# Performance work log

Hardware: AMD Instinct MI355X
Metric: run time of the kernel (lower is better)

## Reference

```python
import jax, jax.numpy as jnp
from jax import lax
import numpy as np

N, D, K, T, E, S = 2048, 128, 16, 16, 8192, 256
GAMMA, SIGMA, TEMP, EPS = 0.1, 1.0, 1.0, 1e-10


def _xavier(k, out_d, in_d):
    lim = (6.0 / (in_d + out_d)) ** 0.5
    return jax.random.uniform(k, (out_d, in_d), minval=-lim, maxval=lim, dtype=jnp.float32)


def setup_inputs() -> dict:
    key = jax.random.key(0)
    ks = jax.random.split(key, 24)
    inp = {
        'edges': jax.random.randint(ks[0], (T, E, 2), 0, N, dtype=jnp.int32),
        'subject_idx': 3,
        'eps_phi': jax.random.normal(ks[1], (T, N, D), dtype=jnp.float32),
        'eps_beta': jax.random.normal(ks[2], (T, K, D), dtype=jnp.float32),
        'u_gumbel': jax.random.uniform(ks[3], (T, 2 * E, K), dtype=jnp.float32),
        'alpha_mean_emb': jax.random.normal(ks[4], (S, D), dtype=jnp.float32),
        'alpha_std_emb': jax.random.normal(ks[5], (S, D), dtype=jnp.float32),
        'W_s2phi': _xavier(ks[6], N * D, D), 'b_s2phi': jnp.zeros((N * D,), jnp.float32),
        'W_s2beta': _xavier(ks[7], K * D, D), 'b_s2beta': jnp.zeros((K * D,), jnp.float32),
        'W_bmean': _xavier(ks[8], D, D), 'b_bmean': jnp.zeros((D,), jnp.float32),
        'W_bstd': _xavier(ks[9], D, D), 'b_bstd': jnp.zeros((D,), jnp.float32),
        'W_pmean': _xavier(ks[10], D, D), 'b_pmean': jnp.zeros((D,), jnp.float32),
        'W_pstd': _xavier(ks[11], D, D), 'b_pstd': jnp.zeros((D,), jnp.float32),
        'W_pi': _xavier(ks[12], K, D),
        'Wih_n': 0.1 * jax.random.normal(ks[13], (3 * D, 2 * D), dtype=jnp.float32),
        'Whh_n': 0.1 * jax.random.normal(ks[14], (3 * D, D), dtype=jnp.float32),
        'bih_n': jnp.zeros((3 * D,), jnp.float32), 'bhh_n': jnp.zeros((3 * D,), jnp.float32),
        'Wih_c': 0.1 * jax.random.normal(ks[15], (3 * D, 2 * D), dtype=jnp.float32),
        'Whh_c': 0.1 * jax.random.normal(ks[16], (3 * D, D), dtype=jnp.float32),
        'bih_c': jnp.zeros((3 * D,), jnp.float32), 'bhh_c': jnp.zeros((3 * D,), jnp.float32),
        'W_dec': _xavier(ks[17], N, D),
    }
    return inp


def _gru(x, h, Wih, Whh, bih, bhh):
    # torch nn.GRU single-step cell (gate order r, z, n)
    gi = x @ Wih.T + bih
    gh = h @ Whh.T + bhh
    i_r, i_z, i_n = jnp.split(gi, 3, axis=-1)
    h_r, h_z, h_n = jnp.split(gh, 3, axis=-1)
    r = jax.nn.sigmoid(i_r + h_r)
    z = jax.nn.sigmoid(i_z + h_z)
    n = jnp.tanh(i_n + r * h_n)
    return (1.0 - z) * n + z * h


def _kld_gauss(m1, s1, m2, s2):
    # KL(N(m1,s1) || N(m2,s2)), s2 scalar
    return 0.5 * jnp.sum(2.0 * (jnp.log(s2) - jnp.log(s1)) + (s1 ** 2 + (m1 - m2) ** 2) / (s2 ** 2) - 1.0)


def reference(edges, subject_idx, eps_phi, eps_beta, u_gumbel,
              alpha_mean_emb, alpha_std_emb, W_s2phi, b_s2phi, W_s2beta, b_s2beta,
              W_bmean, b_bmean, W_bstd, b_bstd, W_pmean, b_pmean, W_pstd, b_pstd,
              W_pi, Wih_n, Whh_n, bih_n, bhh_n, Wih_c, Whh_c, bih_c, bhh_c, W_dec):
    a_m = alpha_mean_emb[subject_idx]
    a_s = jax.nn.softplus(alpha_std_emb[subject_idx])
    kld_alpha = _kld_gauss(a_m, a_s, jnp.zeros_like(a_m), 1.0)
    phi0 = (a_m @ W_s2phi.T + b_s2phi).reshape(N, D)
    beta0 = (a_m @ W_s2beta.T + b_s2beta).reshape(K, D)

    def step(carry, xs):
        h_phi, h_beta, phi_prior, beta_prior = carry
        e_t, ep, eb, u = xs
        w = jnp.concatenate([e_t[:, 0], e_t[:, 1]])  # [2E]
        c = jnp.concatenate([e_t[:, 1], e_t[:, 0]])  # [2E]
        h_phi = _gru(jnp.concatenate([phi_prior, phi_prior], -1), h_phi, Wih_n, Whh_n, bih_n, bhh_n)
        h_beta = _gru(jnp.concatenate([beta_prior, beta_prior], -1), h_beta, Wih_c, Whh_c, bih_c, bhh_c)
        beta_mean = h_beta @ W_bmean.T + b_bmean
        beta_std = jax.nn.softplus(h_beta @ W_bstd.T + b_bstd)
        phi_mean = h_phi @ W_pmean.T + b_pmean
        phi_std = jax.nn.softplus(h_phi @ W_pstd.T + b_pstd)
        beta_s = beta_mean + beta_std * eb  # [K, D]
        phi_s = phi_mean + phi_std * ep     # [N, D]
        logits_q = (phi_s[w] * phi_s[c]) @ W_pi.T        # [2E, K] posterior logits
        log_post = jax.nn.log_softmax(logits_q, axis=-1)
        post = jnp.exp(log_post)
        log_prior = jax.nn.log_softmax(phi_s[w] @ beta_s.T, axis=-1)  # p(z|w)
        g = -jnp.log(-jnp.log(u + EPS) + EPS)  # gumbel noise
        z = jax.nn.softmax((logits_q + g) / TEMP, axis=-1)  # soft gumbel-softmax sample
        recon_logp = jax.nn.log_softmax((z @ beta_s) @ W_dec.T, axis=-1)  # [2E, N]
        nll = -jnp.sum(jnp.take_along_axis(recon_logp, c[:, None], axis=1))
        kld_z = jnp.sum(post * (log_post - log_prior))
        kld_beta = _kld_gauss(beta_mean, beta_std, beta_prior, GAMMA)
        kld_phi = _kld_gauss(phi_mean, phi_std, phi_prior, SIGMA)
        return (h_phi, h_beta, phi_s, beta_s), jnp.stack([nll, kld_z, kld_beta, kld_phi])

    carry0 = (jnp.zeros((N, D), jnp.float32), jnp.zeros((K, D), jnp.float32), phi0, beta0)
    _, per_t = lax.scan(step, carry0, (edges, eps_phi, eps_beta, u_gumbel))
    sums = per_t.sum(axis=0)  # [nll, kld_z, kld_beta, kld_phi]
    cnt = jnp.float32(T * 2 * E)
    out = jnp.stack([sums[0], sums[1], T * kld_alpha, sums[2], sums[3]]) / cnt
    return out  # [nll, kld_z, kld_alpha, kld_beta, kld_phi]
```

## Files before the change

### kernel.cpp

```cpp
#include <hip/hip_runtime.h>

#define NN 2048
#define DD 128
#define KK 16
#define TT 16
#define EE 8192
#define TWOE 16384
#define CNT 262144.0f

#define LOG2E 1.4426950408889634f
#define LN2   0.6931471805599453f

__device__ __forceinline__ float exp2_(float x) { return __builtin_amdgcn_exp2f(x); }
__device__ __forceinline__ float log2_(float x) { return __builtin_amdgcn_logf(x); }
__device__ __forceinline__ float expf_(float x) { return exp2_(x * LOG2E); }
__device__ __forceinline__ float logf_(float x) { return log2_(x) * LN2; }
__device__ __forceinline__ float sigmoidf_(float x) { return 1.f / (1.f + expf_(-x)); }
__device__ __forceinline__ float softplusf_(float x) { return fmaxf(x, 0.f) + logf_(1.f + expf_(-fabsf(x))); }
__device__ __forceinline__ float tanhf_(float x) { return 1.f - 2.f / (1.f + expf_(2.f * x)); }

#define D4(a,b) ((a).x*(b).x + (a).y*(b).y + (a).z*(b).z + (a).w*(b).w)

__launch_bounds__(256)
__global__ void init_kernel(const float* __restrict__ Wih_n, const float* __restrict__ Whh_n,
                            const float* __restrict__ Wih_c, const float* __restrict__ Whh_c,
                            const float* __restrict__ W_pmean, const float* __restrict__ W_pstd,
                            const float* __restrict__ W_bmean, const float* __restrict__ W_bstd,
                            float* __restrict__ Bg_n, float* __restrict__ Bg_c,
                            float* __restrict__ Bms_n, float* __restrict__ Bms_c,
                            float* __restrict__ hphiA, float* __restrict__ hbetaA,
                            const float* __restrict__ amE, const float* __restrict__ asE,
                            const int* __restrict__ sidx, float* __restrict__ acc)
{
    if (blockIdx.x == 1024) {
        __shared__ float red[128];
        int d = threadIdx.x;
        if (d < 128) {
            int s = sidx[0];
            float am = amE[s*128 + d];
            float as = softplusf_(asE[s*128 + d]);
            red[d] = -logf_(as) + 0.5f*(as*as + am*am) - 0.5f;
        }
        __syncthreads();
        for (int st = 64; st > 0; st >>= 1) { if (d < st && d + st < 128) red[d] += red[d + st]; __syncthreads(); }
        if (d == 0) acc[2] = red[0];
        return;
    }
    int idx = blockIdx.x * 256 + threadIdx.x;
    hphiA[idx] = 0.f;
    if (idx < 2048) hbetaA[idx] = 0.f;
    if (idx < 2) { acc[idx] = 0.f; acc[idx + 3] = 0.f; }
    if (idx < 98304) {
        int r = idx;
        if (r < 49152) { int j = r >> 7, k2 = r & 127; Bg_n[r] = Wih_n[j*256 + k2] + Wih_n[j*256 + 128 + k2]; }
        else Bg_n[r] = Whh_n[r - 49152];
    } else if (idx < 196608) {
        int r = idx - 98304;
        if (r < 49152) { int j = r >> 7, k2 = r & 127; Bg_c[r] = Wih_c[j*256 + k2] + Wih_c[j*256 + 128 + k2]; }
        else Bg_c[r] = Whh_c[r - 49152];
    } else if (idx < 229376) {
        int r = idx - 196608;
        Bms_n[r] = (r < 16384) ? W_pmean[r] : W_pstd[r - 16384];
    } else {
        int r = idx - 229376;
        Bms_c[r] = (r < 16384) ? W_bmean[r] : W_bstd[r - 16384];
    }
}

__launch_bounds__(256)
__global__ void phi0_kernel(const float* __restrict__ Wp, const float* __restrict__ bp,
                            const float* __restrict__ Wb, const float* __restrict__ bb,
                            const float* __restrict__ amE, const int* __restrict__ sidx,
                            float* __restrict__ phi0, float* __restrict__ beta0)
{
    int wid = threadIdx.x >> 6, l = threadIdx.x & 63;
    int s = sidx[0];
    long long row = (long long)blockIdx.x * 4 + wid;
    const float* W; const float* b; float* o; long long r = row;
    if (row < 262144) { W = Wp; b = bp; o = phi0; }
    else { W = Wb; b = bb; o = beta0; r = row - 262144; }
    const float* wr = W + r * 128;
    float acc = amE[s*128 + l] * wr[l] + amE[s*128 + 64 + l] * wr[64 + l];
    #pragma unroll
    for (int m = 32; m >= 1; m >>= 1) acc += __shfl_xor(acc, m);
    if (l == 0) o[r] = acc + b[r];
}

__launch_bounds__(256)
__global__ void gru_kernel(const float* __restrict__ phiPrior, const float* __restrict__ betaPrior,
                           const float* __restrict__ hPhiOld, float* __restrict__ hPhiNew,
                           const float* __restrict__ hBetaOld, float* __restrict__ hBetaNew,
                           const float* __restrict__ Bg_n, const float* __restrict__ Bg_c,
                           const float* __restrict__ bih_n, const float* __restrict__ bhh_n,
                           const float* __restrict__ bih_c, const float* __restrict__ bhh_c)
{
    __shared__ float Xs[32][64];
    __shared__ float Hs[32][64];
    __shared__ float Ws[32][192];
    int bx = blockIdx.x;
    const float* X; const float* Hold; float* Hnew; const float* Bg; const float* bih; const float* bhh;
    int m0, M, j0;
    if (bx < 128) {
        m0 = (bx >> 2) * 64; j0 = (bx & 3) * 32; M = 2048;
        X = phiPrior; Hold = hPhiOld; Hnew = hPhiNew; Bg = Bg_n; bih = bih_n; bhh = bhh_n;
    } else {
        m0 = 0; j0 = (bx - 128) * 32; M = 16;
        X = betaPrior; Hold = hBetaOld; Hnew = hBetaNew; Bg = Bg_c; bih = bih_c; bhh = bhh_c;
    }
    int tid = threadIdx.x;
    int j  = tid & 31;
    int rr = tid >> 5;
    float acc[6][8] = {};
    int srow = tid >> 3;
    int skq  = (tid & 7) * 4;
    for (int k0 = 0; k0 < 128; k0 += 32) {
        #pragma unroll
        for (int h2 = 0; h2 < 2; ++h2) {
            int row = srow + 32 * h2;
            int grow = m0 + row;
            float4 xv = make_float4(0.f,0.f,0.f,0.f), hv = xv;
            if (grow < M) {
                xv = *(const float4*)(X    + (size_t)grow*128 + k0 + skq);
                hv = *(const float4*)(Hold + (size_t)grow*128 + k0 + skq);
            }
            Xs[skq+0][row] = xv.x; Xs[skq+1][row] = xv.y; Xs[skq+2][row] = xv.z; Xs[skq+3][row] = xv.w;
            Hs[skq+0][row] = hv.x; Hs[skq+1][row] = hv.y; Hs[skq+2][row] = hv.z; Hs[skq+3][row] = hv.w;
        }
        #pragma unroll
        for (int h6 = 0; h6 < 6; ++h6) {
            int rowIdx = srow + 32 * h6;
            int g = rowIdx >> 5, jj2 = rowIdx & 31;
            float4 wv = *(const float4*)(Bg + (size_t)(g*128 + j0 + jj2)*128 + k0 + skq);
            Ws[skq+0][rowIdx] = wv.x; Ws[skq+1][rowIdx] = wv.y; Ws[skq+2][rowIdx] = wv.z; Ws[skq+3][rowIdx] = wv.w;
        }
        __syncthreads();
        #pragma unroll
        for (int kk = 0; kk < 32; ++kk) {
            float xa[8], ha[8];
            *(float4*)&xa[0] = *(const float4*)&Xs[kk][rr*8];
            *(float4*)&xa[4] = *(const float4*)&Xs[kk][rr*8+4];
            *(float4*)&ha[0] = *(const float4*)&Hs[kk][rr*8];
            *(float4*)&ha[4] = *(const float4*)&Hs[kk][rr*8+4];
            #pragma unroll
            for (int g = 0; g < 3; ++g) {
                float wv = Ws[kk][g*32 + j];
                #pragma unroll
                for (int i = 0; i < 8; ++i) acc[g][i] = fmaf(xa[i], wv, acc[g][i]);
            }
            #pragma unroll
            for (int g = 3; g < 6; ++g) {
                float wv = Ws[kk][g*32 + j];
                #pragma unroll
                for (int i = 0; i < 8; ++i) acc[g][i] = fmaf(ha[i], wv, acc[g][i]);
            }
        }
        __syncthreads();
    }
    float bi_r = bih[j0 + j], bi_z = bih[128 + j0 + j], bi_n = bih[256 + j0 + j];
    float bh_r = bhh[j0 + j], bh_z = bhh[128 + j0 + j], bh_n = bhh[256 + j0 + j];
    #pragma unroll
    for (int i = 0; i < 8; ++i) {
        int row = m0 + rr*8 + i;
        if (row < M) {
            float r_ = sigmoidf_(acc[0][i] + bi_r + acc[3][i] + bh_r);
            float z_ = sigmoidf_(acc[1][i] + bi_z + acc[4][i] + bh_z);
            float n_ = tanhf_(acc[2][i] + bi_n + r_ * (acc[5][i] + bh_n));
            size_t hi = (size_t)row * 128 + j0 + j;
            Hnew[hi] = (1.f - z_) * n_ + z_ * Hold[hi];
        }
    }
}

__launch_bounds__(256)
__global__ void msmt_kernel(const float* __restrict__ hPhi, const float* __restrict__ hBeta,
                            const float* __restrict__ Bms_n, const float* __restrict__ Bms_c,
                            const float* __restrict__ b_pmean, const float* __restrict__ b_pstd,
                            const float* __restrict__ b_bmean, const float* __restrict__ b_bstd,
                            const float* __restrict__ epsP, const float* __restrict__ epsB,
                            const float* __restrict__ phiPrior, const float* __restrict__ betaPrior,
                            float* __restrict__ phiS, float* __restrict__ betaS,
                            const float* __restrict__ W_dec, float* __restrict__ Mt,
                            float* __restrict__ acc)
{
    __shared__ float red[256];
    int bx = blockIdx.x;
    int tid = threadIdx.x;
    if (bx < 128) {
        __shared__ float Hs[32][64];
        __shared__ float Wms[32][64];
        int m0 = (bx >> 2) * 64, j0 = (bx & 3) * 32;
        int j  = tid & 31;
        int rr = tid >> 5;
        float accM[8] = {}, accS[8] = {};
        int srow = tid >> 3;
        int skq  = (tid & 7) * 4;
        for (int k0 = 0; k0 < 128; k0 += 32) {
            #pragma unroll
            for (int h2 = 0; h2 < 2; ++h2) {
                int row = srow + 32 * h2;
                float4 hv = *(const float4*)(hPhi + (size_t)(m0 + row)*128 + k0 + skq);
                Hs[skq+0][row] = hv.x; Hs[skq+1][row] = hv.y; Hs[skq+2][row] = hv.z; Hs[skq+3][row] = hv.w;
            }
            #pragma unroll
            for (int h2 = 0; h2 < 2; ++h2) {
                int ri = srow + 32 * h2;
                int grp = ri >> 5, jj2 = ri & 31;
                float4 wv = *(const float4*)(Bms_n + (size_t)(grp*128 + j0 + jj2)*128 + k0 + skq);
                Wms[skq+0][ri] = wv.x; Wms[skq+1][ri] = wv.y; Wms[skq+2][ri] = wv.z; Wms[skq+3][ri] = wv.w;
            }
            __syncthreads();
            #pragma unroll
            for (int kk = 0; kk < 32; ++kk) {
                float hv[8];
                *(float4*)&hv[0] = *(const float4*)&Hs[kk][rr*8];
                *(float4*)&hv[4] = *(const float4*)&Hs[kk][rr*8+4];
                float wm = Wms[kk][j];
                float wsv = Wms[kk][32 + j];
                #pragma unroll
                for (int i = 0; i < 8; ++i) {
                    accM[i] = fmaf(hv[i], wm, accM[i]);
                    accS[i] = fmaf(hv[i], wsv, accS[i]);
                }
            }
            __syncthreads();
        }
        float bmv = b_pmean[j0 + j], bsv = b_pstd[j0 + j];
        float kld = 0.f;
        #pragma unroll
        for (int i = 0; i < 8; ++i) {
            int row = m0 + rr*8 + i;
            size_t gi = (size_t)row * 128 + j0 + j;
            float mean = accM[i] + bmv;
            float stdv = softplusf_(accS[i] + bsv);
            phiS[gi] = mean + stdv * epsP[gi];
            float d = mean - phiPrior[gi];
            kld += -logf_(stdv) + 0.5f*(stdv*stdv + d*d) - 0.5f;
        }
        red[tid] = kld; __syncthreads();
        for (int st = 128; st > 0; st >>= 1) { if (tid < st) red[tid] += red[tid + st]; __syncthreads(); }
        if (tid == 0) atomicAdd(acc + 4, red[0]);
    } else {
        __shared__ float hb[2048];
        __shared__ float sbeta[16*132];
        int bm = bx - 128;
        {
            int base = tid * 8;
            *(float4*)&hb[base]     = *(const float4*)(hBeta + base);
            *(float4*)&hb[base + 4] = *(const float4*)(hBeta + base + 4);
        }
        __syncthreads();
        {
            int j = tid & 127, half = tid >> 7;
            float accM[8] = {}, accS[8] = {};
            const float* wmrow = Bms_c + (size_t)j * 128;
            const float* wsrow = Bms_c + (size_t)(128 + j) * 128;
            for (int d4 = 0; d4 < 32; ++d4) {
                float4 wm = *(const float4*)(wmrow + d4*4);
                float4 wsv = *(const float4*)(wsrow + d4*4);
                #pragma unroll
                for (int i = 0; i < 8; ++i) {
                    int r = half*8 + i;
                    float4 hv = *(const float4*)&hb[r*128 + d4*4];
                    accM[i] += D4(hv, wm);
                    accS[i] += D4(hv, wsv);
                }
            }
            float bmv = b_bmean[j], bsv = b_bstd[j];
            float kld = 0.f;
            #pragma unroll
            for (int i = 0; i < 8; ++i) {
                int r = half*8 + i;
                float mean = accM[i] + bmv;
                float stdv = softplusf_(accS[i] + bsv);
                float sv = mean + stdv * epsB[r*128 + j];
                sbeta[r*132 + j] = sv;
                if (bm == 0) {
                    betaS[r*128 + j] = sv;
                    float d = mean - betaPrior[r*128 + j];
                    kld += (-2.3025850929940457f - logf_(stdv)) + 50.0f*(stdv*stdv + d*d) - 0.5f;
                }
            }
            if (bm == 0) {
                red[tid] = kld; __syncthreads();
                for (int st = 128; st > 0; st >>= 1) { if (tid < st) red[tid] += red[tid + st]; __syncthreads(); }
                if (tid == 0) atomicAdd(acc + 3, red[0]);
            }
        }
        __syncthreads();
        {
            int w = tid >> 6, l = tid & 63;
            int k = l & 15, q = l >> 4;
            const float* sb = &sbeta[k*132 + q*32];
            #pragma unroll 4
            for (int rr2 = 0; rr2 < 16; ++rr2) {
                int n = bm*64 + w*16 + rr2;
                const float* wd = W_dec + (size_t)n*128 + q*32;
                float p = 0.f;
                #pragma unroll
                for (int i4 = 0; i4 < 8; ++i4) {
                    float4 a = *(const float4*)(sb + i4*4);
                    float4 b = *(const float4*)(wd + i4*4);
                    p += D4(a, b);
                }
                p += __shfl_xor(p, 16);
                p += __shfl_xor(p, 32);
                if (l < 16) Mt[n*16 + l] = p * LOG2E;
            }
        }
    }
}

#define ZSTEP(A,B,Wv,Bv) { float4 a_=(A), b_=(B); \
    lp += a_.x*(Bv).x + a_.y*(Bv).y + a_.z*(Bv).z + a_.w*(Bv).w; \
    lq += (a_.x*b_.x)*(Wv).x + (a_.y*b_.y)*(Wv).y + (a_.z*b_.z)*(Wv).z + (a_.w*b_.w)*(Wv).w; }

__launch_bounds__(512, 2)
__global__ void znll_kernel(const float* __restrict__ phiS, const float* __restrict__ betaS,
                            const float* __restrict__ W_pi, const float* __restrict__ Mt,
                            const int* __restrict__ edges_t, const float* __restrict__ u_t,
                            float* __restrict__ acc)
{
    __shared__ float zbuf[32][16];
    __shared__ int   cbuf[32];
    __shared__ float ss[32][8];
    __shared__ float kred[8], cvred[8];
    int tid = threadIdx.x, wid = tid >> 6, l = tid & 63;
    {
        int k = l >> 2, q = l & 3;
        int d0 = q * 32;
        const float4* wp = (const float4*)(W_pi  + k*128 + d0);
        const float4* bp = (const float4*)(betaS + k*128 + d0);
        float4 wr0 = wp[0], wr1 = wp[1], wr2 = wp[2], wr3 = wp[3],
               wr4 = wp[4], wr5 = wp[5], wr6 = wp[6], wr7 = wp[7];
        float4 br0 = bp[0], br1 = bp[1], br2 = bp[2], br3 = bp[3],
               br4 = bp[4], br5 = bp[5], br6 = bp[6], br7 = bp[7];
        float kz = 0.f;
        #pragma unroll
        for (int it = 0; it < 4; ++it) {
            int jl = wid * 4 + it;
            int j = blockIdx.x * 32 + jl;
            int e = j & 8191; int fl = j >> 13;
            int w = edges_t[e*2 + fl], c = edges_t[e*2 + (fl ^ 1)];
            const float4* pw4 = (const float4*)(phiS + (size_t)w*128 + d0);
            const float4* pc4 = (const float4*)(phiS + (size_t)c*128 + d0);
            float lq = 0.f, lp = 0.f;
            ZSTEP(pw4[0], pc4[0], wr0, br0); ZSTEP(pw4[1], pc4[1], wr1, br1);
            ZSTEP(pw4[2], pc4[2], wr2, br2); ZSTEP(pw4[3], pc4[3], wr3, br3);
            ZSTEP(pw4[4], pc4[4], wr4, br4); ZSTEP(pw4[5], pc4[5], wr5, br5);
            ZSTEP(pw4[6], pc4[6], wr6, br6); ZSTEP(pw4[7], pc4[7], wr7, br7);
            lq += __shfl_xor(lq, 1); lq += __shfl_xor(lq, 2);
            lp += __shfl_xor(lp, 1); lp += __shfl_xor(lp, 2);
            float eq = expf_(lq);
            float sq = eq;
            sq += __shfl_xor(sq, 4); sq += __shfl_xor(sq, 8); sq += __shfl_xor(sq, 16); sq += __shfl_xor(sq, 32);
            float logpost = lq - logf_(sq);
            float post = eq * __builtin_amdgcn_rcpf(sq);
            float mp = lp;
            mp = fmaxf(mp, __shfl_xor(mp, 4));  mp = fmaxf(mp, __shfl_xor(mp, 8));
            mp = fmaxf(mp, __shfl_xor(mp, 16)); mp = fmaxf(mp, __shfl_xor(mp, 32));
            float ep = expf_(lp - mp);
            float sp = ep;
            sp += __shfl_xor(sp, 4); sp += __shfl_xor(sp, 8); sp += __shfl_xor(sp, 16); sp += __shfl_xor(sp, 32);
            float logprior = (lp - mp) - logf_(sp);
            kz += post * (logpost - logprior);
            float u = u_t[(size_t)j*16 + k];
            float g = -logf_(-logf_(u + 1e-10f) + 1e-10f);
            float zl = lq + g;
            float ez = expf_(zl);
            float sz = ez;
            sz += __shfl_xor(sz, 4); sz += __shfl_xor(sz, 8); sz += __shfl_xor(sz, 16); sz += __shfl_xor(sz, 32);
            if (q == 0) zbuf[jl][k] = ez * __builtin_amdgcn_rcpf(sz);
            if (l == 0) cbuf[jl] = c;
        }
        #pragma unroll
        for (int m = 1; m < 64; m <<= 1) kz += __shfl_xor(kz, m);
        if (l == 0) kred[wid] = kz * 0.25f;
    }
    __syncthreads();
    int n0 = tid * 4;
    const float4* mp4 = (const float4*)(Mt + (size_t)n0 * 16);
    float4 M0 = mp4[0],  M1 = mp4[1],  M2 = mp4[2],  M3 = mp4[3];
    float4 M4 = mp4[4],  M5 = mp4[5],  M6 = mp4[6],  M7 = mp4[7];
    float4 M8 = mp4[8],  M9 = mp4[9],  M10 = mp4[10], M11 = mp4[11];
    float4 M12 = mp4[12], M13 = mp4[13], M14 = mp4[14], M15 = mp4[15];
    float cvsum = 0.f;
    #pragma unroll 2
    for (int e = 0; e < 32; ++e) {
        const float4* zp = (const float4*)&zbuf[e][0];
        float4 Z0 = zp[0], Z1 = zp[1], Z2 = zp[2], Z3 = zp[3];
        int c = cbuf[e];
        float v0 = D4(Z0, M0)  + D4(Z1, M1)  + D4(Z2, M2)  + D4(Z3, M3);
        float v1 = D4(Z0, M4)  + D4(Z1, M5)  + D4(Z2, M6)  + D4(Z3, M7);
        float v2 = D4(Z0, M8)  + D4(Z1, M9)  + D4(Z2, M10) + D4(Z3, M11);
        float v3 = D4(Z0, M12) + D4(Z1, M13) + D4(Z2, M14) + D4(Z3, M15);
        float s = exp2_(v0) + exp2_(v1) + exp2_(v2) + exp2_(v3);
        cvsum += (c == n0) ? v0 : 0.f;
        cvsum += (c == n0 + 1) ? v1 : 0.f;
        cvsum += (c == n0 + 2) ? v2 : 0.f;
        cvsum += (c == n0 + 3) ? v3 : 0.f;
        #pragma unroll
        for (int m = 1; m < 64; m <<= 1) s += __shfl_xor(s, m);
        if (l == 0) ss[e][wid] = s;
    }
    #pragma unroll
    for (int m = 1; m < 64; m <<= 1) cvsum += __shfl_xor(cvsum, m);
    if (l == 0) cvred[wid] = cvsum;
    __syncthreads();
    if (wid == 0) {
        float val = 0.f;
        if (l < 32) {
            float S = 0.f;
            #pragma unroll
            for (int w2 = 0; w2 < 8; ++w2) S += ss[l][w2];
            val = log2_(S);
        }
        #pragma unroll
        for (int m = 1; m < 64; m <<= 1) val += __shfl_xor(val, m);
        if (l == 0) {
            float cvt = 0.f, kzt = 0.f;
            #pragma unroll
            for (int w2 = 0; w2 < 8; ++w2) { cvt += cvred[w2]; kzt += kred[w2]; }
            atomicAdd(acc + 0, LN2 * (val - cvt));
            atomicAdd(acc + 1, kzt);
        }
    }
}

__global__ void final_kernel(const float* __restrict__ acc, float* __restrict__ out)
{
    if (threadIdx.x == 0 && blockIdx.x == 0) {
        out[0] = acc[0] / CNT;
        out[1] = acc[1] / CNT;
        out[2] = 16.f * acc[2] / CNT;
        out[3] = acc[3] / CNT;
        out[4] = acc[4] / CNT;
    }
}

extern "C" void kernel_launch(void* const* d_in, const int* in_sizes, int n_in,
                              void* d_out, int out_size, void* d_ws, size_t ws_size,
                              hipStream_t stream)
{
    (void)in_sizes; (void)n_in; (void)out_size; (void)ws_size;
    const int*   edges   = (const int*)d_in[0];
    const int*   sidx    = (const int*)d_in[1];
    const float* eps_phi = (const float*)d_in[2];
    const float* eps_beta= (const float*)d_in[3];
    const float* u_g     = (const float*)d_in[4];
    const float* amE     = (const float*)d_in[5];
    const float* asE     = (const float*)d_in[6];
    const float* W_s2phi = (const float*)d_in[7];
    const float* b_s2phi = (const float*)d_in[8];
    const float* W_s2beta= (const float*)d_in[9];
    const float* b_s2beta= (const float*)d_in[10];
    const float* W_bmean = (const float*)d_in[11];
    const float* b_bmean = (const float*)d_in[12];
    const float* W_bstd  = (const float*)d_in[13];
    const float* b_bstd  = (const float*)d_in[14];
    const float* W_pmean = (const float*)d_in[15];
    const float* b_pmean = (const float*)d_in[16];
    const float* W_pstd  = (const float*)d_in[17];
    const float* b_pstd  = (const float*)d_in[18];
    const float* W_pi    = (const float*)d_in[19];
    const float* Wih_n   = (const float*)d_in[20];
    const float* Whh_n   = (const float*)d_in[21];
    const float* bih_n   = (const float*)d_in[22];
    const float* bhh_n   = (const float*)d_in[23];
    const float* Wih_c   = (const float*)d_in[24];
    const float* Whh_c   = (const float*)d_in[25];
    const float* bih_c   = (const float*)d_in[26];
    const float* bhh_c   = (const float*)d_in[27];
    const float* W_dec   = (const float*)d_in[28];

    float* ws     = (float*)d_ws;
    float* Bg_n   = ws;
    float* Bg_c   = Bg_n   + 98304;
    float* Bms_n  = Bg_c   + 98304;
    float* Bms_c  = Bms_n  + 32768;
    float* phiA   = Bms_c  + 32768;
    float* phiB   = phiA   + 262144;
    float* hphiA  = phiB   + 262144;
    float* hphiB  = hphiA  + 262144;
    float* betaA  = hphiB  + 262144;
    float* betaB  = betaA  + 2048;
    float* hbetaA = betaB  + 2048;
    float* hbetaB = hbetaA + 2048;
    float* Mt     = hbetaB + 2048;
    float* acc    = Mt     + 32768;

    init_kernel<<<1025, 256, 0, stream>>>(Wih_n, Whh_n, Wih_c, Whh_c,
                                          W_pmean, W_pstd, W_bmean, W_bstd,
                                          Bg_n, Bg_c, Bms_n, Bms_c,
                                          hphiA, hbetaA, amE, asE, sidx, acc);
    phi0_kernel<<<66048, 256, 0, stream>>>(W_s2phi, b_s2phi, W_s2beta, b_s2beta, amE, sidx, phiA, betaA);

    float* phiPrior = phiA;  float* phiS = phiB;
    float* betaPrior = betaA; float* betaS = betaB;
    float* hPhiOld = hphiA;  float* hPhiNew = hphiB;
    float* hBetaOld = hbetaA; float* hBetaNew = hbetaB;
    for (int t = 0; t < TT; ++t) {
        gru_kernel<<<132, 256, 0, stream>>>(phiPrior, betaPrior,
                                            hPhiOld, hPhiNew, hBetaOld, hBetaNew,
                                            Bg_n, Bg_c, bih_n, bhh_n, bih_c, bhh_c);
        msmt_kernel<<<160, 256, 0, stream>>>(hPhiNew, hBetaNew, Bms_n, Bms_c,
                                             b_pmean, b_pstd, b_bmean, b_bstd,
                                             eps_phi + (size_t)t * 262144, eps_beta + (size_t)t * 2048,
                                             phiPrior, betaPrior, phiS, betaS, W_dec, Mt, acc);
        znll_kernel<<<512, 512, 0, stream>>>(phiS, betaS, W_pi, Mt,
                                             edges + (size_t)t * EE * 2, u_g + (size_t)t * TWOE * KK, acc);
        float* tp = phiPrior; phiPrior = phiS; phiS = tp;
        float* tb = betaPrior; betaPrior = betaS; betaS = tb;
        float* th = hPhiOld; hPhiOld = hPhiNew; hPhiNew = th;
        float* tb2 = hBetaOld; hBetaOld = hBetaNew; hBetaNew = tb2;
    }
    final_kernel<<<1, 64, 0, stream>>>(acc, (float*)d_out);
}
```

Baseline: 2.471 ms.

## Split fused z/nll kernel into separate z and nll kernels via global Z buffer

Splits the fused kernel into two. The first kernel computes the gumbel-softmax z samples and the KL(z) term and writes Z to a global buffer. The second loads Z per 64-edge tile and computes the reconstruction log-softmax against all 2048 nodes. Each nll block now covers twice as many edges, so the 64-register Mt load per thread is amortised better, and the z phase runs with smaller blocks and higher occupancy. The cost is an extra launch per timestep and a Z round-trip through global memory.

```diff
diff --git a/kernel.cpp b/kernel.cpp
--- a/kernel.cpp
+++ b/kernel.cpp
@@ -314,79 +314,97 @@
     lp += a_.x*(Bv).x + a_.y*(Bv).y + a_.z*(Bv).z + a_.w*(Bv).w; \
     lq += (a_.x*b_.x)*(Wv).x + (a_.y*b_.y)*(Wv).y + (a_.z*b_.z)*(Wv).z + (a_.w*b_.w)*(Wv).w; }
 
+__launch_bounds__(256, 3)
+__global__ void z_kernel(const float* __restrict__ phiS, const float* __restrict__ betaS,
+                         const float* __restrict__ W_pi, const int* __restrict__ edges_t,
+                         const float* __restrict__ u_t, float* __restrict__ Z,
+                         float* __restrict__ acc)
+{
+    __shared__ float kred[4];
+    int tid = threadIdx.x, wid = tid >> 6, l = tid & 63;
+    int k = l >> 2, q = l & 3;
+    int d0 = q * 32;
+    const float4* wp = (const float4*)(W_pi  + k*128 + d0);
+    const float4* bp = (const float4*)(betaS + k*128 + d0);
+    float4 wr0 = wp[0], wr1 = wp[1], wr2 = wp[2], wr3 = wp[3],
+           wr4 = wp[4], wr5 = wp[5], wr6 = wp[6], wr7 = wp[7];
+    float4 br0 = bp[0], br1 = bp[1], br2 = bp[2], br3 = bp[3],
+           br4 = bp[4], br5 = bp[5], br6 = bp[6], br7 = bp[7];
+    float kz = 0.f;
+    int gw = blockIdx.x * 4 + wid;
+    #pragma unroll
+    for (int it = 0; it < 4; ++it) {
+        int j = gw * 4 + it;
+        int e = j & 8191; int fl = j >> 13;
+        int w = edges_t[e*2 + fl], c = edges_t[e*2 + (fl ^ 1)];
+        const float4* pw4 = (const float4*)(phiS + (size_t)w*128 + d0);
+        const float4* pc4 = (const float4*)(phiS + (size_t)c*128 + d0);
+        float lq = 0.f, lp = 0.f;
+        ZSTEP(pw4[0], pc4[0], wr0, br0); ZSTEP(pw4[1], pc4[1], wr1, br1);
+        ZSTEP(pw4[2], pc4[2], wr2, br2); ZSTEP(pw4[3], pc4[3], wr3, br3);
+        ZSTEP(pw4[4], pc4[4], wr4, br4); ZSTEP(pw4[5], pc4[5], wr5, br5);
+        ZSTEP(pw4[6], pc4[6], wr6, br6); ZSTEP(pw4[7], pc4[7], wr7, br7);
+        lq += __shfl_xor(lq, 1); lq += __shfl_xor(lq, 2);
+        lp += __shfl_xor(lp, 1); lp += __shfl_xor(lp, 2);
+        float eq = expf_(lq);
+        float sq = eq;
+        sq += __shfl_xor(sq, 4); sq += __shfl_xor(sq, 8); sq += __shfl_xor(sq, 16); sq += __shfl_xor(sq, 32);
+        float logpost = lq - logf_(sq);
+        float post = eq * __builtin_amdgcn_rcpf(sq);
+        float mp = lp;
+        mp = fmaxf(mp, __shfl_xor(mp, 4));  mp = fmaxf(mp, __shfl_xor(mp, 8));
+        mp = fmaxf(mp, __shfl_xor(mp, 16)); mp = fmaxf(mp, __shfl_xor(mp, 32));
+        float ep = expf_(lp - mp);
+        float sp = ep;
+        sp += __shfl_xor(sp, 4); sp += __shfl_xor(sp, 8); sp += __shfl_xor(sp, 16); sp += __shfl_xor(sp, 32);
+        float logprior = (lp - mp) - logf_(sp);
+        kz += post * (logpost - logprior);
+        float u = u_t[(size_t)j*16 + k];
+        float g = -logf_(-logf_(u + 1e-10f) + 1e-10f);
+        float zl = lq + g;
+        float ez = expf_(zl);
+        float sz = ez;
+        sz += __shfl_xor(sz, 4); sz += __shfl_xor(sz, 8); sz += __shfl_xor(sz, 16); sz += __shfl_xor(sz, 32);
+        if (q == 0) Z[(size_t)j*16 + k] = ez * __builtin_amdgcn_rcpf(sz);
+    }
+    #pragma unroll
+    for (int m = 1; m < 64; m <<= 1) kz += __shfl_xor(kz, m);
+    if (l == 0) kred[wid] = kz * 0.25f;
+    __syncthreads();
+    if (tid == 0) atomicAdd(acc + 1, kred[0] + kred[1] + kred[2] + kred[3]);
+}
+
 __launch_bounds__(512, 2)
-__global__ void znll_kernel(const float* __restrict__ phiS, const float* __restrict__ betaS,
-                            const float* __restrict__ W_pi, const float* __restrict__ Mt,
-                            const int* __restrict__ edges_t, const float* __restrict__ u_t,
-                            float* __restrict__ acc)
-{
-    __shared__ float zbuf[32][16];
-    __shared__ int   cbuf[32];
-    __shared__ float ss[32][8];
-    __shared__ float kred[8], cvred[8];
+__global__ void nll_kernel(const float* __restrict__ Mt, const float* __restrict__ Z,
+                           const int* __restrict__ edges_t, float* __restrict__ acc)
+{
+    __shared__ float zs[64][16];
+    __shared__ int   cbuf[64];
+    __shared__ float ss[64][8];
+    __shared__ float cvred[8];
     int tid = threadIdx.x, wid = tid >> 6, l = tid & 63;
-    {
-        int k = l >> 2, q = l & 3;
-        int d0 = q * 32;
-        const float4* wp = (const float4*)(W_pi  + k*128 + d0);
-        const float4* bp = (const float4*)(betaS + k*128 + d0);
-        float4 wr0 = wp[0], wr1 = wp[1], wr2 = wp[2], wr3 = wp[3],
-               wr4 = wp[4], wr5 = wp[5], wr6 = wp[6], wr7 = wp[7];
-        float4 br0 = bp[0], br1 = bp[1], br2 = bp[2], br3 = bp[3],
-               br4 = bp[4], br5 = bp[5], br6 = bp[6], br7 = bp[7];
-        float kz = 0.f;
-        #pragma unroll
-        for (int it = 0; it < 4; ++it) {
-            int jl = wid * 4 + it;
-            int j = blockIdx.x * 32 + jl;
-            int e = j & 8191; int fl = j >> 13;
-            int w = edges_t[e*2 + fl], c = edges_t[e*2 + (fl ^ 1)];
-            const float4* pw4 = (const float4*)(phiS + (size_t)w*128 + d0);
-            const float4* pc4 = (const float4*)(phiS + (size_t)c*128 + d0);
-            float lq = 0.f, lp = 0.f;
-            ZSTEP(pw4[0], pc4[0], wr0, br0); ZSTEP(pw4[1], pc4[1], wr1, br1);
-            ZSTEP(pw4[2], pc4[2], wr2, br2); ZSTEP(pw4[3], pc4[3], wr3, br3);
-            ZSTEP(pw4[4], pc4[4], wr4, br4); ZSTEP(pw4[5], pc4[5], wr5, br5);
-            ZSTEP(pw4[6], pc4[6], wr6, br6); ZSTEP(pw4[7], pc4[7], wr7, br7);
-            lq += __shfl_xor(lq, 1); lq += __shfl_xor(lq, 2);
-            lp += __shfl_xor(lp, 1); lp += __shfl_xor(lp, 2);
-            float eq = expf_(lq);
-            float sq = eq;
-            sq += __shfl_xor(sq, 4); sq += __shfl_xor(sq, 8); sq += __shfl_xor(sq, 16); sq += __shfl_xor(sq, 32);
-            float logpost = lq - logf_(sq);
-            float post = eq * __builtin_amdgcn_rcpf(sq);
-            float mp = lp;
-            mp = fmaxf(mp, __shfl_xor(mp, 4));  mp = fmaxf(mp, __shfl_xor(mp, 8));
-            mp = fmaxf(mp, __shfl_xor(mp, 16)); mp = fmaxf(mp, __shfl_xor(mp, 32));
-            float ep = expf_(lp - mp);
-            float sp = ep;
-            sp += __shfl_xor(sp, 4); sp += __shfl_xor(sp, 8); sp += __shfl_xor(sp, 16); sp += __shfl_xor(sp, 32);
-            float logprior = (lp - mp) - logf_(sp);
-            kz += post * (logpost - logprior);
-            float u = u_t[(size_t)j*16 + k];
-            float g = -logf_(-logf_(u + 1e-10f) + 1e-10f);
-            float zl = lq + g;
-            float ez = expf_(zl);
-            float sz = ez;
-            sz += __shfl_xor(sz, 4); sz += __shfl_xor(sz, 8); sz += __shfl_xor(sz, 16); sz += __shfl_xor(sz, 32);
-            if (q == 0) zbuf[jl][k] = ez * __builtin_amdgcn_rcpf(sz);
-            if (l == 0) cbuf[jl] = c;
-        }
-        #pragma unroll
-        for (int m = 1; m < 64; m <<= 1) kz += __shfl_xor(kz, m);
-        if (l == 0) kred[wid] = kz * 0.25f;
-    }
-    __syncthreads();
+    int j0 = blockIdx.x * 64;
+    if (tid < 256) {
+        int e = tid >> 2, f4 = tid & 3;
+        *(float4*)&zs[e][f4*4] = *(const float4*)(Z + (size_t)(j0 + e)*16 + f4*4);
+    }
+    if (tid >= 256 && tid < 320) {
+        int jl = tid - 256;
+        int j = j0 + jl;
+        int e = j & 8191; int fl = j >> 13;
+        cbuf[jl] = edges_t[e*2 + (fl ^ 1)];
+    }
     int n0 = tid * 4;
     const float4* mp4 = (const float4*)(Mt + (size_t)n0 * 16);
     float4 M0 = mp4[0],  M1 = mp4[1],  M2 = mp4[2],  M3 = mp4[3];
     float4 M4 = mp4[4],  M5 = mp4[5],  M6 = mp4[6],  M7 = mp4[7];
     float4 M8 = mp4[8],  M9 = mp4[9],  M10 = mp4[10], M11 = mp4[11];
     float4 M12 = mp4[12], M13 = mp4[13], M14 = mp4[14], M15 = mp4[15];
+    __syncthreads();
     float cvsum = 0.f;
     #pragma unroll 2
-    for (int e = 0; e < 32; ++e) {
-        const float4* zp = (const float4*)&zbuf[e][0];
+    for (int e = 0; e < 64; ++e) {
+        const float4* zp = (const float4*)&zs[e][0];
         float4 Z0 = zp[0], Z1 = zp[1], Z2 = zp[2], Z3 = zp[3];
         int c = cbuf[e];
         float v0 = D4(Z0, M0)  + D4(Z1, M1)  + D4(Z2, M2)  + D4(Z3, M3);
@@ -407,21 +425,17 @@
     if (l == 0) cvred[wid] = cvsum;
     __syncthreads();
     if (wid == 0) {
-        float val = 0.f;
-        if (l < 32) {
-            float S = 0.f;
-            #pragma unroll
-            for (int w2 = 0; w2 < 8; ++w2) S += ss[l][w2];
-            val = log2_(S);
-        }
+        float S = 0.f;
+        #pragma unroll
+        for (int w2 = 0; w2 < 8; ++w2) S += ss[l][w2];
+        float val = log2_(S);
         #pragma unroll
         for (int m = 1; m < 64; m <<= 1) val += __shfl_xor(val, m);
         if (l == 0) {
-            float cvt = 0.f, kzt = 0.f;
-            #pragma unroll
-            for (int w2 = 0; w2 < 8; ++w2) { cvt += cvred[w2]; kzt += kred[w2]; }
+            float cvt = 0.f;
+            #pragma unroll
+            for (int w2 = 0; w2 < 8; ++w2) cvt += cvred[w2];
             atomicAdd(acc + 0, LN2 * (val - cvt));
-            atomicAdd(acc + 1, kzt);
         }
     }
 }
@@ -486,7 +500,8 @@
     float* hbetaA = betaB  + 2048;
     float* hbetaB = hbetaA + 2048;
     float* Mt     = hbetaB + 2048;
-    float* acc    = Mt     + 32768;
+    float* Zb     = Mt     + 32768;
+    float* acc    = Zb     + 262144;
 
     init_kernel<<<1025, 256, 0, stream>>>(Wih_n, Whh_n, Wih_c, Whh_c,
                                           W_pmean, W_pstd, W_bmean, W_bstd,
@@ -506,8 +521,9 @@
                                              b_pmean, b_pstd, b_bmean, b_bstd,
                                              eps_phi + (size_t)t * 262144, eps_beta + (size_t)t * 2048,
                                              phiPrior, betaPrior, phiS, betaS, W_dec, Mt, acc);
-        znll_kernel<<<512, 512, 0, stream>>>(phiS, betaS, W_pi, Mt,
-                                             edges + (size_t)t * EE * 2, u_g + (size_t)t * TWOE * KK, acc);
+        z_kernel<<<1024, 256, 0, stream>>>(phiS, betaS, W_pi,
+                                           edges + (size_t)t * EE * 2, u_g + (size_t)t * TWOE * KK, Zb, acc);
+        nll_kernel<<<256, 512, 0, stream>>>(Mt, Zb, edges + (size_t)t * EE * 2, acc);
         float* tp = phiPrior; phiPrior = phiS; phiS = tp;
         float* tb = betaPrior; betaPrior = betaS; betaS = tb;
         float* th = hPhiOld; hPhiOld = hPhiNew; hPhiNew = th;
```

Measured after the change: 2.455 ms. Within noise of the previous version (-0.6%).
